# Optimization experiments

Hardware: AMD Instinct MI355X
Metric: run time of the kernel (lower is better)

Reference implementation:

```python
import jax, jax.numpy as jnp
import numpy as np

EPS = 1e-5

def _layernorm(x, g, b):
    m = jnp.mean(x, axis=-1, keepdims=True)
    v = jnp.var(x, axis=-1, keepdims=True)
    return (x - m) * jax.lax.rsqrt(v + EPS) * g + b

def setup_inputs() -> dict:
    key = jax.random.key(0)
    ks = jax.random.split(key, 8)
    B, N, D, H = 4, 2048, 1024, 16
    F = 2 * D
    s = 0.02
    return {
        "x": jax.random.normal(ks[0], (B, N, D), jnp.float32),
        "mask": jnp.zeros((B, N, N), jnp.float32),
        "Wq": jax.random.normal(ks[1], (D, D), jnp.float32) * s,
        "Wk": jax.random.normal(ks[2], (D, D), jnp.float32) * s,
        "Wv": jax.random.normal(ks[3], (D, D), jnp.float32) * s,
        "Wc": jax.random.normal(ks[4], (D, D), jnp.float32) * s,
        "bc": jnp.zeros((D,), jnp.float32),
        "W1": jax.random.normal(ks[5], (D, F), jnp.float32) * s,
        "b1": jnp.zeros((F,), jnp.float32),
        "W2": jax.random.normal(ks[6], (F, D), jnp.float32) * s,
        "b2": jnp.zeros((D,), jnp.float32),
        "g1": jnp.ones((D,), jnp.float32),
        "be1": jnp.zeros((D,), jnp.float32),
        "g2": jnp.ones((D,), jnp.float32),
        "be2": jnp.zeros((D,), jnp.float32),
    }

def reference(x, mask, Wq, Wk, Wv, Wc, bc, W1, b1, W2, b2, g1, be1, g2, be2):
    B, N, D = x.shape
    H = 16
    Dh = D // H
    scale = 1.0 / np.sqrt(Dh).astype(np.float32)
    # projections -> [B, H, N, Dh]
    def heads(t):
        return t.reshape(B, N, H, Dh).transpose(0, 2, 1, 3)
    q = heads(x @ Wq)
    k = heads(x @ Wk)
    v = heads(x @ Wv)
    score = jnp.einsum('bhnd,bhmd->bhnm', q, k) * scale + mask[:, None, :, :]
    attn = jnp.einsum('bhnm,bhmd->bhnd', jax.nn.softmax(score, axis=-1), v)
    attn = attn.transpose(0, 2, 1, 3).reshape(B, N, D)
    x = x + attn @ Wc + bc
    x = _layernorm(x, g1, be1)
    x = x + jnp.maximum(x @ W1 + b1, 0.0) @ W2 + b2
    x = _layernorm(x, g2, be2)
    return x
```

## Files before the change

kernel.cpp:

```cpp
#include <hip/hip_runtime.h>
#include <hip/hip_bf16.h>


#define DEV __device__ __forceinline__

using s16x8 = __attribute__((ext_vector_type(8))) short;
using f32x4 = __attribute__((ext_vector_type(4))) float;

DEV unsigned short f2bf(float f) {
  unsigned u = __float_as_uint(f);
  u += 0x7fffu + ((u >> 16) & 1u);
  return (unsigned short)(u >> 16);
}
DEV unsigned cvt_pk_bf16(float lo, float hi) {
  unsigned r;
  asm("v_cvt_pk_bf16_f32 %0, %1, %2" : "=v"(r) : "v"(lo), "v"(hi));
  return r;
}
DEV float bf2f(unsigned short b) { return __uint_as_float((unsigned)b << 16); }

typedef __attribute__((address_space(3))) unsigned lds_u32_t;
typedef const __attribute__((address_space(1))) unsigned glb_u32_t;

DEV void gld_lds16(const void* g, void* l) {
  __builtin_amdgcn_global_load_lds((glb_u32_t*)g, (lds_u32_t*)l, 16, 0, 0);
}

template<int RELU, int VOUT>
__global__ __launch_bounds__(512, 2)
void gemm8p(const unsigned short* __restrict__ A, const unsigned short* __restrict__ Bt,
            unsigned short* __restrict__ Cb, const float* __restrict__ bias,
            unsigned short* __restrict__ vtout, int M, int N, int K)
{
  __shared__ unsigned short Sh[2][2][256 * 64];
  const int tid = threadIdx.x;
  const int w = tid >> 6, lane = tid & 63;
  const int g = lane >> 4, q = lane & 15;
  const int wr = w >> 2, wc = w & 3;

  const int nwg  = gridDim.x * gridDim.y;
  const int flat = blockIdx.y * gridDim.x + blockIdx.x;
  const int rm   = (flat & 7) * (nwg >> 3) + (flat >> 3);
  const int m0 = (rm / gridDim.x) * 256, n0 = (rm % gridDim.x) * 256;

  f32x4 acc[8][4] = {};

  const int srow = w * 8 + (lane >> 3);
  const int scol = ((lane & 7) ^ (lane >> 3)) * 8;
  const unsigned short* Ag = A  + (size_t)(m0 + srow) * K + scol;
  const unsigned short* Bg = Bt + (size_t)(n0 + srow) * K + scol;

  auto STG = [&](const unsigned short* Gb, int buf, int ab, int half, int kt) {
    const unsigned short* gs = Gb + (size_t)(half * 128) * K + kt * 64;
    unsigned short* ls = &Sh[buf][ab][(half * 128 + w * 8) * 64];
    gld_lds16(gs, ls);
    gld_lds16(gs + (size_t)64 * K, ls + 64 * 64);
  };
  auto LDA = [&](int buf, int mq, s16x8 af[4][2]) {
#pragma unroll
    for (int mm = 0; mm < 4; ++mm) {
      const unsigned short* rp = &Sh[buf][0][(wr * 128 + mq * 64 + mm * 16 + q) * 64];
#pragma unroll
      for (int kk = 0; kk < 2; ++kk)
        af[mm][kk] = *(const s16x8*)(rp + (((kk * 4 + g) ^ (q & 7)) * 8));
    }
  };
  auto LDB = [&](int buf, int nq, s16x8 bf[2][2]) {
#pragma unroll
    for (int nn = 0; nn < 2; ++nn) {
      const unsigned short* rp = &Sh[buf][1][(wc * 64 + nq * 32 + nn * 16 + q) * 64];
#pragma unroll
      for (int kk = 0; kk < 2; ++kk)
        bf[nn][kk] = *(const s16x8*)(rp + (((kk * 4 + g) ^ (q & 7)) * 8));
    }
  };
  auto MQ = [&](int mq, int nq, const s16x8 af[4][2], const s16x8 bf[2][2]) {
    __builtin_amdgcn_s_setprio(1);
#pragma unroll
    for (int kk = 0; kk < 2; ++kk)
#pragma unroll
      for (int mm = 0; mm < 4; ++mm)
#pragma unroll
        for (int nn = 0; nn < 2; ++nn)
          acc[mq * 4 + mm][nq * 2 + nn] = __builtin_amdgcn_mfma_f32_16x16x32_bf16(
              af[mm][kk], bf[nn][kk], acc[mq * 4 + mm][nq * 2 + nn], 0, 0, 0);
    __builtin_amdgcn_s_setprio(0);
  };
  auto BAR = [&]() { __builtin_amdgcn_sched_barrier(0); __builtin_amdgcn_s_barrier(); };

  STG(Ag, 0, 0, 0, 0); STG(Ag, 0, 0, 1, 0);
  STG(Bg, 0, 1, 0, 0); STG(Bg, 0, 1, 1, 0);

  const int NKT = K >> 6;
  s16x8 af[4][2], bf0[2][2], bf1[2][2];
#pragma unroll 1
  for (int kt = 0; kt < NKT; ++kt) {
    const int b = kt & 1, sb = b ^ 1, kn = kt + 1;
    const bool stg = (kn < NKT);
    if (stg) { STG(Ag, sb, 0, 0, kn); asm volatile("s_waitcnt vmcnt(2)" ::: "memory"); }
    else     {                        asm volatile("s_waitcnt vmcnt(0)" ::: "memory"); }
    BAR();
    LDA(b, 0, af); LDB(b, 0, bf0);
    MQ(0, 0, af, bf0);
    BAR();
    if (stg) STG(Ag, sb, 0, 1, kn);
    LDB(b, 1, bf1);
    MQ(0, 1, af, bf1);
    BAR();
    if (stg) STG(Bg, sb, 1, 0, kn);
    LDA(b, 1, af);
    MQ(1, 0, af, bf0);
    BAR();
    if (stg) STG(Bg, sb, 1, 1, kn);
    MQ(1, 1, af, bf1);
    BAR();
  }

#pragma unroll
  for (int n = 0; n < 4; ++n) {
    const int col = n0 + wc * 64 + n * 16 + q;
    if (VOUT && col >= 2048) {
      const int cv = col - 2048;
#pragma unroll
      for (int m = 0; m < 8; ++m) {
        const int row0 = m0 + wr * 128 + m * 16 + g * 4;
        const int bb = row0 >> 11;
        ushort4 pk;
        pk.x = f2bf(acc[m][n][0]); pk.y = f2bf(acc[m][n][1]);
        pk.z = f2bf(acc[m][n][2]); pk.w = f2bf(acc[m][n][3]);
        *(ushort4*)(vtout + ((size_t)bb * 1024 + cv) * 2048 + (row0 & 2047)) = pk;
      }
    } else {
      const float scl = (VOUT && col < 1024) ? 0.18033688011112042f : 1.0f;
      const float bv = bias ? bias[col] : 0.0f;
#pragma unroll
      for (int m = 0; m < 8; ++m) {
        const int row0 = m0 + wr * 128 + m * 16 + g * 4;
#pragma unroll
        for (int r = 0; r < 4; ++r) {
          float v = acc[m][n][r] * scl + bv;
          if (RELU) v = fmaxf(v, 0.0f);
          Cb[(size_t)(row0 + r) * N + col] = f2bf(v);
        }
      }
    }
  }
}

template<int RELU, int RESID, int OUTF>
__global__ __launch_bounds__(256)
void gemm_bt(const unsigned short* __restrict__ A, const unsigned short* __restrict__ Bt,
             unsigned short* __restrict__ Cb, float* __restrict__ Cf,
             const float* __restrict__ bias, const float* __restrict__ resid,
             const unsigned short* __restrict__ residb,
             int M, int N, int K)
{
  __shared__ unsigned short As[128 * 32];
  __shared__ unsigned short Bs[128 * 32];
  const int tid  = threadIdx.x;
  const int wave = tid >> 6, lane = tid & 63;
  const int g = lane >> 4, q = lane & 15;

  const int nwg  = gridDim.x * gridDim.y;
  const int flat = blockIdx.y * gridDim.x + blockIdx.x;
  const int rm   = (nwg & 7) ? flat : ((flat & 7) * (nwg >> 3) + (flat >> 3));
  const int m0 = (rm / gridDim.x) * 128, n0 = (rm % gridDim.x) * 128;
  const int wr = wave >> 1, wc = wave & 1;

  f32x4 acc[4][4] = {};

  const int i0 = wave * 512 + lane * 8;
  const int i1 = 2048 + i0;

  for (int kt = 0; kt < K; kt += 32) {
    gld_lds16(A  + (size_t)(m0 + (i0 >> 5)) * K + kt + (i0 & 31), As + wave * 512);
    gld_lds16(Bt + (size_t)(n0 + (i0 >> 5)) * K + kt + (i0 & 31), Bs + wave * 512);
    gld_lds16(A  + (size_t)(m0 + (i1 >> 5)) * K + kt + (i1 & 31), As + 2048 + wave * 512);
    gld_lds16(Bt + (size_t)(n0 + (i1 >> 5)) * K + kt + (i1 & 31), Bs + 2048 + wave * 512);
    __syncthreads();
    s16x8 a[4], b[4];
#pragma unroll
    for (int m = 0; m < 4; ++m)
      a[m] = *(const s16x8*)(As + (wr * 64 + m * 16 + q) * 32 + g * 8);
#pragma unroll
    for (int n = 0; n < 4; ++n)
      b[n] = *(const s16x8*)(Bs + (wc * 64 + n * 16 + q) * 32 + g * 8);
#pragma unroll
    for (int m = 0; m < 4; ++m)
#pragma unroll
      for (int n = 0; n < 4; ++n)
        acc[m][n] = __builtin_amdgcn_mfma_f32_16x16x32_bf16(a[m], b[n], acc[m][n], 0, 0, 0);
    __syncthreads();
  }

#pragma unroll
  for (int n = 0; n < 4; ++n) {
    const int col = n0 + wc * 64 + n * 16 + q;
    const float bv = bias ? bias[col] : 0.0f;
#pragma unroll
    for (int m = 0; m < 4; ++m) {
      const int row0 = m0 + wr * 64 + m * 16 + g * 4;
#pragma unroll
      for (int r = 0; r < 4; ++r) {
        float v = acc[m][n][r] + bv;
        if (RELU) v = fmaxf(v, 0.0f);
        if (RESID == 1) v += resid[(size_t)(row0 + r) * N + col];
        if (RESID == 2) v += bf2f(residb[(size_t)(row0 + r) * N + col]);
        if (OUTF) Cf[(size_t)(row0 + r) * N + col] = v;
        else      Cb[(size_t)(row0 + r) * N + col] = f2bf(v);
      }
    }
  }
}

__global__ __launch_bounds__(256, 4)
void attn_kernel(const unsigned short* __restrict__ qkv,
                 const unsigned short* __restrict__ vt,
                 const float* __restrict__ mask,
                 unsigned short* __restrict__ outb)
{
  __shared__ unsigned short Ks[2][4096];
  __shared__ unsigned short Vs[2][4096];
  __shared__ unsigned short Pl[4][1024];
  const int tid = threadIdx.x, wave = tid >> 6, lane = tid & 63;
  const int g = lane >> 4, q = lane & 15;

  const int flat = blockIdx.y * 32 + blockIdx.x;
  const int rm   = (flat & 7) * 256 + (flat >> 3);
  const int qt = rm & 31, bh = rm >> 5;
  const int b = bh >> 4, h = bh & 15;
  const int qrow = qt * 64 + wave * 16;
  const size_t tok0 = (size_t)b * 2048;

  const unsigned short* Qp = qkv + (tok0 + qrow + q) * 3072 + h * 64;
  const s16x8 bq0 = *(const s16x8*)(Qp + g * 8);
  const s16x8 bq1 = *(const s16x8*)(Qp + 32 + g * 8);
  const float* Mp = mask + ((size_t)b * 2048 + qrow + q) * 2048;

  const int lr = lane >> 3;
  const int sc = (lane & 7) ^ lr;
  const unsigned short* Kg = qkv + tok0 * 3072 + 1024 + h * 64
                           + (size_t)(wave * 16 + lr) * 3072 + sc * 8;
  const unsigned short* Vg = vt + ((size_t)bh * 64 + wave * 16 + lr) * 2048 + sc * 8;
  unsigned short* KsW = Ks[0] + wave * 1024;
  unsigned short* VsW = Vs[0] + wave * 1024;

  auto STAGE = [&](int buf, int t) {
    const size_t ko = (size_t)t * (64 * 3072);
    const int    vo = t * 64;
    gld_lds16(Kg + ko,            KsW + buf * 4096);
    gld_lds16(Kg + ko + 8 * 3072, KsW + buf * 4096 + 512);
    gld_lds16(Vg + vo,            VsW + buf * 4096);
    gld_lds16(Vg + vo + 8 * 2048, VsW + buf * 4096 + 512);
  };

  s16x8 ones;
#pragma unroll
  for (int j = 0; j < 8; ++j) ones[j] = (short)0x3F80;

  f32x4 ot[4] = {};
  f32x4 sacc = {};
  f32x4 mkc[4], mkn[4];
  float m = -3.0e38f;
  char* Pw = (char*)&Pl[wave][0];
  const float L2E = 1.4426950408889634f;
  const float THR = 11.541560327111707f;

  STAGE(0, 0);
#pragma unroll
  for (int m2 = 0; m2 < 4; ++m2) mkc[m2] = *(const f32x4*)(Mp + m2 * 16 + g * 4);
  __syncthreads();

  int cur = 0;
#pragma unroll 1
  for (int t = 0; t < 32; ++t) {
    if (t < 31) {
      STAGE(cur ^ 1, t + 1);
#pragma unroll
      for (int m2 = 0; m2 < 4; ++m2)
        mkn[m2] = *(const f32x4*)(Mp + (t + 1) * 64 + m2 * 16 + g * 4);
    }
    const unsigned short* Kt = Ks[cur];
    const unsigned short* Vt = Vs[cur];

    f32x4 st[4] = {};
    __builtin_amdgcn_s_setprio(1);
#pragma unroll
    for (int m2 = 0; m2 < 4; ++m2) {
      const unsigned short* kp = Kt + (m2 * 16 + q) * 64;
      const s16x8 ak0 = *(const s16x8*)(kp + ((g       ^ (q & 7)) * 8));
      const s16x8 ak1 = *(const s16x8*)(kp + (((g + 4) ^ (q & 7)) * 8));
      st[m2] = __builtin_amdgcn_mfma_f32_16x16x32_bf16(ak0, bq0, st[m2], 0, 0, 0);
      st[m2] = __builtin_amdgcn_mfma_f32_16x16x32_bf16(ak1, bq1, st[m2], 0, 0, 0);
    }
    __builtin_amdgcn_s_setprio(0);

#pragma unroll
    for (int m2 = 0; m2 < 4; ++m2)
#pragma unroll
      for (int r = 0; r < 4; ++r)
        st[m2][r] = fmaf(mkc[m2][r], L2E, st[m2][r]);

    float c0 = fmaxf(fmaxf(fmaxf(st[0][0], st[0][1]), st[0][2]), st[0][3]);
    float c1 = fmaxf(fmaxf(fmaxf(st[1][0], st[1][1]), st[1][2]), st[1][3]);
    float c2 = fmaxf(fmaxf(fmaxf(st[2][0], st[2][1]), st[2][2]), st[2][3]);
    float c3 = fmaxf(fmaxf(fmaxf(st[3][0], st[3][1]), st[3][2]), st[3][3]);
    float tmax = fmaxf(fmaxf(fmaxf(c0, c1), c2), c3);
    tmax = fmaxf(tmax, __shfl_xor(tmax, 16));
    tmax = fmaxf(tmax, __shfl_xor(tmax, 32));

    if (!__all(tmax <= m + THR)) {
      const float mn = fmaxf(m, tmax);
      const float al = exp2f(m - mn);
      m = mn;
      sacc[0] *= al;
#pragma unroll
      for (int mm = 0; mm < 4; ++mm) {
        ot[mm][0] *= al; ot[mm][1] *= al; ot[mm][2] *= al; ot[mm][3] *= al;
      }
    }

#pragma unroll
    for (int m2 = 0; m2 < 4; ++m2) {
#pragma unroll
      for (int r = 0; r < 4; ++r)
        st[m2][r] = exp2f(st[m2][r] - m);
      const int bir  = m2 * 32 + g * 8;
      const int addr = q * 128 + (((bir >> 4) ^ (q & 7)) << 4) + (bir & 15);
      uint2 pk;
      pk.x = cvt_pk_bf16(st[m2][0], st[m2][1]);
      pk.y = cvt_pk_bf16(st[m2][2], st[m2][3]);
      *(uint2*)(Pw + addr) = pk;
    }

    __builtin_amdgcn_s_setprio(1);
#pragma unroll
    for (int kb = 0; kb < 2; ++kb) {
      const int blk = (kb * 4 + g) ^ (q & 7);
      const s16x8 pb = *(const s16x8*)(Pw + q * 128 + blk * 16);
      sacc = __builtin_amdgcn_mfma_f32_16x16x32_bf16(ones, pb, sacc, 0, 0, 0);
#pragma unroll
      for (int mm = 0; mm < 4; ++mm) {
        const s16x8 av = *(const s16x8*)(Vt + (mm * 16 + q) * 64 + blk * 8);
        ot[mm] = __builtin_amdgcn_mfma_f32_16x16x32_bf16(av, pb, ot[mm], 0, 0, 0);
      }
    }
    __builtin_amdgcn_s_setprio(0);

#pragma unroll
    for (int m2 = 0; m2 < 4; ++m2) mkc[m2] = mkn[m2];
    __syncthreads();
    cur ^= 1;
  }

  const float inv = 1.0f / sacc[0];
#pragma unroll
  for (int mm = 0; mm < 4; ++mm) {
    const int bir  = mm * 32 + g * 8;
    const int addr = q * 128 + (((bir >> 4) ^ (q & 7)) << 4) + (bir & 15);
    uint2 pk;
    pk.x = cvt_pk_bf16(ot[mm][0] * inv, ot[mm][1] * inv);
    pk.y = cvt_pk_bf16(ot[mm][2] * inv, ot[mm][3] * inv);
    *(uint2*)(Pw + addr) = pk;
  }
#pragma unroll
  for (int p = 0; p < 2; ++p) {
    const int c  = p * 64 + lane;
    const int qq = c >> 3, cc = c & 7;
    const int blk = cc ^ (qq & 7);
    const s16x8 vv = *(const s16x8*)(Pw + qq * 128 + blk * 16);
    *(s16x8*)(outb + (tok0 + qrow + qq) * 1024 + h * 64 + cc * 8) = vv;
  }
}

template<int INBF>
__global__ __launch_bounds__(256)
void ln_kernel(const float* __restrict__ inf, const unsigned short* __restrict__ inb,
               float* __restrict__ outf, unsigned short* __restrict__ outb,
               const float* __restrict__ gam, const float* __restrict__ bet)
{
  __shared__ float red[8];
  const int row = blockIdx.x, tid = threadIdx.x;
  f32x4 v;
  if (INBF) {
    const uint2 u = *(const uint2*)(inb + (size_t)row * 1024 + tid * 4);
    v[0] = __uint_as_float(u.x << 16); v[1] = __uint_as_float(u.x & 0xffff0000u);
    v[2] = __uint_as_float(u.y << 16); v[3] = __uint_as_float(u.y & 0xffff0000u);
  } else {
    v = *(const f32x4*)(inf + (size_t)row * 1024 + tid * 4);
  }
  float s  = v[0] + v[1] + v[2] + v[3];
  float ss = v[0]*v[0] + v[1]*v[1] + v[2]*v[2] + v[3]*v[3];
#pragma unroll
  for (int o = 1; o < 64; o <<= 1) { s += __shfl_xor(s, o); ss += __shfl_xor(ss, o); }
  if ((tid & 63) == 0) { red[tid >> 6] = s; red[4 + (tid >> 6)] = ss; }
  __syncthreads();
  s  = red[0] + red[1] + red[2] + red[3];
  ss = red[4] + red[5] + red[6] + red[7];
  const float mean = s * (1.0f / 1024.0f);
  const float var  = ss * (1.0f / 1024.0f) - mean * mean;
  const float rstd = rsqrtf(var + 1e-5f);
  const f32x4 gm = *(const f32x4*)(gam + tid * 4);
  const f32x4 bt = *(const f32x4*)(bet + tid * 4);
  f32x4 o;
#pragma unroll
  for (int j = 0; j < 4; ++j) o[j] = (v[j] - mean) * rstd * gm[j] + bt[j];
  if (outf) *(f32x4*)(outf + (size_t)row * 1024 + tid * 4) = o;
  if (outb) {
    uint2 pk; pk.x = cvt_pk_bf16(o[0], o[1]); pk.y = cvt_pk_bf16(o[2], o[3]);
    *(uint2*)(outb + (size_t)row * 1024 + tid * 4) = pk;
  }
}

__global__ __launch_bounds__(256)
void tcast_kernel(const float* __restrict__ in, unsigned short* __restrict__ out, int R, int C)
{
  __shared__ float t[32][33];
  const int tx = threadIdx.x & 31, ty = threadIdx.x >> 5;
  const int c0 = blockIdx.x * 32, r0 = blockIdx.y * 32;
#pragma unroll
  for (int k = 0; k < 4; ++k)
    t[ty + k * 8][tx] = in[(size_t)(r0 + ty + k * 8) * C + c0 + tx];
  __syncthreads();
#pragma unroll
  for (int k = 0; k < 4; ++k)
    out[(size_t)(c0 + ty + k * 8) * R + r0 + tx] = f2bf(t[tx][ty + k * 8]);
}

__global__ __launch_bounds__(256)
void cast_x_kernel(const float* __restrict__ in, unsigned short* __restrict__ out)
{
  const size_t i = ((size_t)blockIdx.x * 256 + threadIdx.x) * 4;
  const f32x4 v = *(const f32x4*)(in + i);
  uint2 pk; pk.x = cvt_pk_bf16(v[0], v[1]); pk.y = cvt_pk_bf16(v[2], v[3]);
  *(uint2*)(out + i) = pk;
}

extern "C" void kernel_launch(void* const* d_in, const int* in_sizes, int n_in,
                              void* d_out, int out_size, void* d_ws, size_t ws_size,
                              hipStream_t stream)
{
  (void)in_sizes; (void)n_in; (void)out_size; (void)ws_size;
  const float* x   = (const float*)d_in[0];
  const float* msk = (const float*)d_in[1];
  const float* Wq  = (const float*)d_in[2];
  const float* Wk  = (const float*)d_in[3];
  const float* Wv  = (const float*)d_in[4];
  const float* Wc  = (const float*)d_in[5];
  const float* bc  = (const float*)d_in[6];
  const float* W1  = (const float*)d_in[7];
  const float* b1  = (const float*)d_in[8];
  const float* W2  = (const float*)d_in[9];
  const float* b2  = (const float*)d_in[10];
  const float* g1  = (const float*)d_in[11];
  const float* be1 = (const float*)d_in[12];
  const float* g2  = (const float*)d_in[13];
  const float* be2 = (const float*)d_in[14];
  float* out = (float*)d_out;
  char* ws = (char*)d_ws;
  const size_t MB = 1u << 20;
  unsigned short* xb    = (unsigned short*)(ws + 0 * MB);
  unsigned short* wqkvt = (unsigned short*)(ws + 16 * MB);
  unsigned short* wct   = (unsigned short*)(ws + 22 * MB);
  unsigned short* w1t   = (unsigned short*)(ws + 24 * MB);
  unsigned short* w2t   = (unsigned short*)(ws + 28 * MB);
  unsigned short* qkv   = (unsigned short*)(ws + 32 * MB);
  unsigned short* vt    = (unsigned short*)(ws + 80 * MB);
  unsigned short* attnb = (unsigned short*)(ws + 96 * MB);
  unsigned short* y1b   = (unsigned short*)(ws + 112 * MB);
  unsigned short* midb  = (unsigned short*)(ws + 32 * MB);
  unsigned short* z2b   = (unsigned short*)(ws + 64 * MB);
  unsigned short* h1b   = (unsigned short*)(ws + 128 * MB);

  cast_x_kernel<<<8192, 256, 0, stream>>>(x, xb);
  tcast_kernel<<<dim3(32, 32), 256, 0, stream>>>(Wq, wqkvt,               1024, 1024);
  tcast_kernel<<<dim3(32, 32), 256, 0, stream>>>(Wk, wqkvt + 1024 * 1024, 1024, 1024);
  tcast_kernel<<<dim3(32, 32), 256, 0, stream>>>(Wv, wqkvt + 2048 * 1024, 1024, 1024);
  tcast_kernel<<<dim3(32, 32), 256, 0, stream>>>(Wc, wct,                 1024, 1024);
  tcast_kernel<<<dim3(64, 32), 256, 0, stream>>>(W1, w1t,                 1024, 2048);
  tcast_kernel<<<dim3(32, 64), 256, 0, stream>>>(W2, w2t,                 2048, 1024);

  gemm8p<0, 1><<<dim3(12, 32), 512, 0, stream>>>(xb, wqkvt, qkv, nullptr, vt,
                                                 8192, 3072, 1024);
  attn_kernel<<<dim3(32, 64), 256, 0, stream>>>(qkv, vt, msk, attnb);
  gemm_bt<0, 2, 0><<<dim3(8, 64), 256, 0, stream>>>(attnb, wct, y1b, nullptr,
                                                    bc, nullptr, xb, 8192, 1024, 1024);
  ln_kernel<1><<<8192, 256, 0, stream>>>(nullptr, y1b, nullptr, h1b, g1, be1);
  gemm8p<1, 0><<<dim3(8, 32), 512, 0, stream>>>(h1b, w1t, midb, b1, nullptr,
                                                8192, 2048, 1024);
  gemm_bt<0, 2, 0><<<dim3(8, 64), 256, 0, stream>>>(midb, w2t, z2b, nullptr,
                                                    b2, nullptr, h1b, 8192, 1024, 2048);
  ln_kernel<1><<<8192, 256, 0, stream>>>(nullptr, z2b, out, nullptr, g2, be2);
}
```

Baseline: 432.1 us.

## Rewrite attention with 32x32x16 MFMA and register-resident P via permlane swap

Moves the attention kernel from 16x16x32 to 32x32x16 MFMA tiles, so each wave handles 32 query rows and a block handles 128 rows, which halves the grid. The probability tile stays in registers, rearranged with v_permlane32_swap instead of going through an LDS round-trip, and the output is written straight from registers. This cuts LDS traffic and doubles K/V reuse per staged tile. In exchange it uses more registers (occupancy hint lowered from 4 to 3) and drops the mask prefetch one tile ahead.

```diff
diff --git a/kernel.cpp b/kernel.cpp
--- a/kernel.cpp
+++ b/kernel.cpp
@@ -4,8 +4,9 @@
 
 #define DEV __device__ __forceinline__
 
-using s16x8 = __attribute__((ext_vector_type(8))) short;
-using f32x4 = __attribute__((ext_vector_type(4))) float;
+using s16x8  = __attribute__((ext_vector_type(8))) short;
+using f32x4  = __attribute__((ext_vector_type(4))) float;
+using f32x16 = __attribute__((ext_vector_type(16))) float;
 
 DEV unsigned short f2bf(float f) {
   unsigned u = __float_as_uint(f);
@@ -213,7 +214,7 @@
   }
 }
 
-__global__ __launch_bounds__(256, 4)
+__global__ __launch_bounds__(256, 3)
 void attn_kernel(const unsigned short* __restrict__ qkv,
                  const unsigned short* __restrict__ vt,
                  const float* __restrict__ mask,
@@ -221,21 +222,23 @@
 {
   __shared__ unsigned short Ks[2][4096];
   __shared__ unsigned short Vs[2][4096];
-  __shared__ unsigned short Pl[4][1024];
   const int tid = threadIdx.x, wave = tid >> 6, lane = tid & 63;
-  const int g = lane >> 4, q = lane & 15;
-
-  const int flat = blockIdx.y * 32 + blockIdx.x;
-  const int rm   = (flat & 7) * 256 + (flat >> 3);
-  const int qt = rm & 31, bh = rm >> 5;
+  const int q32 = lane & 31, hi = lane >> 5;
+
+  const int flat = blockIdx.y * 16 + blockIdx.x;
+  const int rm   = (flat & 7) * 128 + (flat >> 3);
+  const int qt = rm & 15, bh = rm >> 4;
   const int b = bh >> 4, h = bh & 15;
-  const int qrow = qt * 64 + wave * 16;
+  const int qrow = qt * 128 + wave * 32;
   const size_t tok0 = (size_t)b * 2048;
 
-  const unsigned short* Qp = qkv + (tok0 + qrow + q) * 3072 + h * 64;
-  const s16x8 bq0 = *(const s16x8*)(Qp + g * 8);
-  const s16x8 bq1 = *(const s16x8*)(Qp + 32 + g * 8);
-  const float* Mp = mask + ((size_t)b * 2048 + qrow + q) * 2048;
+  s16x8 bq[4];
+  {
+    const unsigned short* Qp = qkv + (tok0 + qrow + q32) * 3072 + h * 64 + hi * 8;
+#pragma unroll
+    for (int s = 0; s < 4; ++s) bq[s] = *(const s16x8*)(Qp + s * 16);
+  }
+  const float* Mp = mask + ((size_t)b * 2048 + qrow + q32) * 2048;
 
   const int lr = lane >> 3;
   const int sc = (lane & 7) ^ lr;
@@ -258,118 +261,117 @@
 #pragma unroll
   for (int j = 0; j < 8; ++j) ones[j] = (short)0x3F80;
 
-  f32x4 ot[4] = {};
-  f32x4 sacc = {};
-  f32x4 mkc[4], mkn[4];
+  f32x16 ot0 = {}, ot1 = {}, sacc = {};
   float m = -3.0e38f;
-  char* Pw = (char*)&Pl[wave][0];
   const float L2E = 1.4426950408889634f;
   const float THR = 11.541560327111707f;
+  const int swz = lane & 7;
 
   STAGE(0, 0);
-#pragma unroll
-  for (int m2 = 0; m2 < 4; ++m2) mkc[m2] = *(const f32x4*)(Mp + m2 * 16 + g * 4);
   __syncthreads();
 
   int cur = 0;
 #pragma unroll 1
   for (int t = 0; t < 32; ++t) {
-    if (t < 31) {
-      STAGE(cur ^ 1, t + 1);
-#pragma unroll
-      for (int m2 = 0; m2 < 4; ++m2)
-        mkn[m2] = *(const f32x4*)(Mp + (t + 1) * 64 + m2 * 16 + g * 4);
-    }
+    if (t < 31) STAGE(cur ^ 1, t + 1);
     const unsigned short* Kt = Ks[cur];
     const unsigned short* Vt = Vs[cur];
 
-    f32x4 st[4] = {};
+    f32x16 st0, st1;
+#pragma unroll
+    for (int bb = 0; bb < 4; ++bb) {
+      const f32x4 m0 = *(const f32x4*)(Mp + t * 64 +      8 * bb + 4 * hi);
+      const f32x4 m1 = *(const f32x4*)(Mp + t * 64 + 32 + 8 * bb + 4 * hi);
+#pragma unroll
+      for (int i = 0; i < 4; ++i) {
+        st0[bb * 4 + i] = m0[i] * L2E;
+        st1[bb * 4 + i] = m1[i] * L2E;
+      }
+    }
+
     __builtin_amdgcn_s_setprio(1);
 #pragma unroll
-    for (int m2 = 0; m2 < 4; ++m2) {
-      const unsigned short* kp = Kt + (m2 * 16 + q) * 64;
-      const s16x8 ak0 = *(const s16x8*)(kp + ((g       ^ (q & 7)) * 8));
-      const s16x8 ak1 = *(const s16x8*)(kp + (((g + 4) ^ (q & 7)) * 8));
-      st[m2] = __builtin_amdgcn_mfma_f32_16x16x32_bf16(ak0, bq0, st[m2], 0, 0, 0);
-      st[m2] = __builtin_amdgcn_mfma_f32_16x16x32_bf16(ak1, bq1, st[m2], 0, 0, 0);
+    for (int s = 0; s < 4; ++s) {
+      const int ch = (((2 * s + hi) ^ swz)) * 8;
+      const s16x8 ak0 = *(const s16x8*)(Kt + q32 * 64 + ch);
+      const s16x8 ak1 = *(const s16x8*)(Kt + (32 + q32) * 64 + ch);
+      st0 = __builtin_amdgcn_mfma_f32_32x32x16_bf16(ak0, bq[s], st0, 0, 0, 0);
+      st1 = __builtin_amdgcn_mfma_f32_32x32x16_bf16(ak1, bq[s], st1, 0, 0, 0);
     }
     __builtin_amdgcn_s_setprio(0);
 
-#pragma unroll
-    for (int m2 = 0; m2 < 4; ++m2)
-#pragma unroll
-      for (int r = 0; r < 4; ++r)
-        st[m2][r] = fmaf(mkc[m2][r], L2E, st[m2][r]);
-
-    float c0 = fmaxf(fmaxf(fmaxf(st[0][0], st[0][1]), st[0][2]), st[0][3]);
-    float c1 = fmaxf(fmaxf(fmaxf(st[1][0], st[1][1]), st[1][2]), st[1][3]);
-    float c2 = fmaxf(fmaxf(fmaxf(st[2][0], st[2][1]), st[2][2]), st[2][3]);
-    float c3 = fmaxf(fmaxf(fmaxf(st[3][0], st[3][1]), st[3][2]), st[3][3]);
-    float tmax = fmaxf(fmaxf(fmaxf(c0, c1), c2), c3);
-    tmax = fmaxf(tmax, __shfl_xor(tmax, 16));
-    tmax = fmaxf(tmax, __shfl_xor(tmax, 32));
-
-    if (!__all(tmax <= m + THR)) {
-      const float mn = fmaxf(m, tmax);
+    float x0 = fmaxf(fmaxf(st0[0],  st0[1]),  fmaxf(st0[2],  st0[3]));
+    float x1 = fmaxf(fmaxf(st0[4],  st0[5]),  fmaxf(st0[6],  st0[7]));
+    float x2 = fmaxf(fmaxf(st0[8],  st0[9]),  fmaxf(st0[10], st0[11]));
+    float x3 = fmaxf(fmaxf(st0[12], st0[13]), fmaxf(st0[14], st0[15]));
+    float y0 = fmaxf(fmaxf(st1[0],  st1[1]),  fmaxf(st1[2],  st1[3]));
+    float y1 = fmaxf(fmaxf(st1[4],  st1[5]),  fmaxf(st1[6],  st1[7]));
+    float y2 = fmaxf(fmaxf(st1[8],  st1[9]),  fmaxf(st1[10], st1[11]));
+    float y3 = fmaxf(fmaxf(st1[12], st1[13]), fmaxf(st1[14], st1[15]));
+    float tmax = fmaxf(fmaxf(fmaxf(x0, x1), fmaxf(x2, x3)),
+                       fmaxf(fmaxf(y0, y1), fmaxf(y2, y3)));
+    const float rmax = fmaxf(tmax, __shfl_xor(tmax, 32));
+
+    if (!__all(rmax <= m + THR)) {
+      const float mn = fmaxf(m, rmax);
       const float al = exp2f(m - mn);
       m = mn;
-      sacc[0] *= al;
-#pragma unroll
-      for (int mm = 0; mm < 4; ++mm) {
-        ot[mm][0] *= al; ot[mm][1] *= al; ot[mm][2] *= al; ot[mm][3] *= al;
+#pragma unroll
+      for (int r = 0; r < 16; ++r) { sacc[r] *= al; ot0[r] *= al; ot1[r] *= al; }
+    }
+
+#pragma unroll
+    for (int r = 0; r < 16; ++r) {
+      st0[r] = exp2f(st0[r] - m);
+      st1[r] = exp2f(st1[r] - m);
+    }
+
+    unsigned pw[4][4];
+#pragma unroll
+    for (int sg = 0; sg < 2; ++sg) {
+#pragma unroll
+      for (int w = 0; w < 2; ++w) {
+        unsigned A0 = cvt_pk_bf16(st0[8*sg + 2*w],     st0[8*sg + 2*w + 1]);
+        unsigned B0 = cvt_pk_bf16(st0[8*sg + 4 + 2*w], st0[8*sg + 5 + 2*w]);
+        asm("v_permlane32_swap_b32 %0, %1" : "+v"(B0), "+v"(A0));
+        pw[sg][w] = A0; pw[sg][2 + w] = B0;
+        unsigned A1 = cvt_pk_bf16(st1[8*sg + 2*w],     st1[8*sg + 2*w + 1]);
+        unsigned B1 = cvt_pk_bf16(st1[8*sg + 4 + 2*w], st1[8*sg + 5 + 2*w]);
+        asm("v_permlane32_swap_b32 %0, %1" : "+v"(B1), "+v"(A1));
+        pw[2 + sg][w] = A1; pw[2 + sg][2 + w] = B1;
       }
     }
 
-#pragma unroll
-    for (int m2 = 0; m2 < 4; ++m2) {
-#pragma unroll
-      for (int r = 0; r < 4; ++r)
-        st[m2][r] = exp2f(st[m2][r] - m);
-      const int bir  = m2 * 32 + g * 8;
-      const int addr = q * 128 + (((bir >> 4) ^ (q & 7)) << 4) + (bir & 15);
-      uint2 pk;
-      pk.x = cvt_pk_bf16(st[m2][0], st[m2][1]);
-      pk.y = cvt_pk_bf16(st[m2][2], st[m2][3]);
-      *(uint2*)(Pw + addr) = pk;
-    }
-
     __builtin_amdgcn_s_setprio(1);
 #pragma unroll
-    for (int kb = 0; kb < 2; ++kb) {
-      const int blk = (kb * 4 + g) ^ (q & 7);
-      const s16x8 pb = *(const s16x8*)(Pw + q * 128 + blk * 16);
-      sacc = __builtin_amdgcn_mfma_f32_16x16x32_bf16(ones, pb, sacc, 0, 0, 0);
-#pragma unroll
-      for (int mm = 0; mm < 4; ++mm) {
-        const s16x8 av = *(const s16x8*)(Vt + (mm * 16 + q) * 64 + blk * 8);
-        ot[mm] = __builtin_amdgcn_mfma_f32_16x16x32_bf16(av, pb, ot[mm], 0, 0, 0);
-      }
+    for (int s = 0; s < 4; ++s) {
+      union { unsigned u[4]; s16x8 v; } cv;
+      cv.u[0] = pw[s][0]; cv.u[1] = pw[s][1]; cv.u[2] = pw[s][2]; cv.u[3] = pw[s][3];
+      const s16x8 pb = cv.v;
+      const int ch = (((2 * s + hi) ^ swz)) * 8;
+      const s16x8 av0 = *(const s16x8*)(Vt + q32 * 64 + ch);
+      const s16x8 av1 = *(const s16x8*)(Vt + (32 + q32) * 64 + ch);
+      sacc = __builtin_amdgcn_mfma_f32_32x32x16_bf16(ones, pb, sacc, 0, 0, 0);
+      ot0  = __builtin_amdgcn_mfma_f32_32x32x16_bf16(av0,  pb, ot0,  0, 0, 0);
+      ot1  = __builtin_amdgcn_mfma_f32_32x32x16_bf16(av1,  pb, ot1,  0, 0, 0);
     }
     __builtin_amdgcn_s_setprio(0);
 
-#pragma unroll
-    for (int m2 = 0; m2 < 4; ++m2) mkc[m2] = mkn[m2];
     __syncthreads();
     cur ^= 1;
   }
 
   const float inv = 1.0f / sacc[0];
-#pragma unroll
-  for (int mm = 0; mm < 4; ++mm) {
-    const int bir  = mm * 32 + g * 8;
-    const int addr = q * 128 + (((bir >> 4) ^ (q & 7)) << 4) + (bir & 15);
-    uint2 pk;
-    pk.x = cvt_pk_bf16(ot[mm][0] * inv, ot[mm][1] * inv);
-    pk.y = cvt_pk_bf16(ot[mm][2] * inv, ot[mm][3] * inv);
-    *(uint2*)(Pw + addr) = pk;
-  }
-#pragma unroll
-  for (int p = 0; p < 2; ++p) {
-    const int c  = p * 64 + lane;
-    const int qq = c >> 3, cc = c & 7;
-    const int blk = cc ^ (qq & 7);
-    const s16x8 vv = *(const s16x8*)(Pw + qq * 128 + blk * 16);
-    *(s16x8*)(outb + (tok0 + qrow + qq) * 1024 + h * 64 + cc * 8) = vv;
+  unsigned short* orow = outb + (tok0 + qrow + q32) * 1024 + h * 64 + hi * 4;
+#pragma unroll
+  for (int bb = 0; bb < 4; ++bb) {
+    uint2 p0, p1;
+    p0.x = cvt_pk_bf16(ot0[4*bb]     * inv, ot0[4*bb + 1] * inv);
+    p0.y = cvt_pk_bf16(ot0[4*bb + 2] * inv, ot0[4*bb + 3] * inv);
+    p1.x = cvt_pk_bf16(ot1[4*bb]     * inv, ot1[4*bb + 1] * inv);
+    p1.y = cvt_pk_bf16(ot1[4*bb + 2] * inv, ot1[4*bb + 3] * inv);
+    *(uint2*)(orow + 8 * bb)      = p0;
+    *(uint2*)(orow + 32 + 8 * bb) = p1;
   }
 }
 
@@ -482,7 +484,7 @@
 
   gemm8p<0, 1><<<dim3(12, 32), 512, 0, stream>>>(xb, wqkvt, qkv, nullptr, vt,
                                                  8192, 3072, 1024);
-  attn_kernel<<<dim3(32, 64), 256, 0, stream>>>(qkv, vt, msk, attnb);
+  attn_kernel<<<dim3(16, 64), 256, 0, stream>>>(qkv, vt, msk, attnb);
   gemm_bt<0, 2, 0><<<dim3(8, 64), 256, 0, stream>>>(attnb, wct, y1b, nullptr,
                                                     bc, nullptr, xb, 8192, 1024, 1024);
   ln_kernel<1><<<8192, 256, 0, stream>>>(nullptr, y1b, nullptr, h1b, g1, be1);
```

Measured after the change: 442.9 us. 1.02x slower.
